# Optimization experiments

Hardware: AMD Instinct MI355X
Metric: run time of the kernel (lower is better)

## Reference

```python
import jax, jax.numpy as jnp
import numpy as np

B, S, D = 2, 2048, 2048
H, HKV, HD = 16, 2, 128
THETA = 10000.0


def setup_inputs() -> dict:
    key = jax.random.key(0)
    ks = jax.random.split(key, 5)
    x = jax.random.normal(ks[0], (B, S, D), jnp.float32)
    Wq = jax.random.normal(ks[1], (D, H * HD), jnp.float32) * 0.02
    Wk = jax.random.normal(ks[2], (D, HKV * HD), jnp.float32) * 0.02
    Wv = jax.random.normal(ks[3], (D, HKV * HD), jnp.float32) * 0.02
    Wo = jax.random.normal(ks[4], (H * HD, D), jnp.float32) * 0.02
    mask = jnp.tril(jnp.ones((S, S), jnp.int32))[None, None]  # causal [1,1,S,S]
    return {"x": x, "mask": mask, "Wq": Wq, "Wk": Wk, "Wv": Wv, "Wo": Wo}


def _rope(t, seq_len):
    # t: [B, S, H, HD]; matches RotaryPositionalEmbedding (cos/sin broadcast [S,1,HD])
    inv_freq = 1.0 / (THETA ** (jnp.arange(0, HD, 2, dtype=jnp.float32) / HD))
    pos = jnp.arange(seq_len, dtype=jnp.float32)
    freqs = jnp.einsum('i,j->ij', pos, inv_freq)          # [S, HD/2]
    emb = jnp.concatenate([freqs, freqs], axis=-1)        # [S, HD]
    cos = jnp.cos(emb)[:, None, :]
    sin = jnp.sin(emb)[:, None, :]
    x1, x2 = jnp.split(t, 2, axis=-1)
    rot = jnp.concatenate([-x2, x1], axis=-1)             # rotate_half
    return t * cos + rot * sin


def reference(x, mask, Wq, Wk, Wv, Wo):
    Bx, Sx, _ = x.shape
    q = (x @ Wq).reshape(Bx, Sx, H, HD)
    k = (x @ Wk).reshape(Bx, Sx, HKV, HD)
    v = (x @ Wv).reshape(Bx, Sx, HKV, HD)
    q = _rope(q, Sx)
    k = _rope(k, Sx)
    rep = H // HKV
    # torch .repeat along head dim == tiling (not interleaved)
    k = jnp.tile(k, (1, 1, rep, 1))  # [B, S, H, HD]
    v = jnp.tile(v, (1, 1, rep, 1))
    scale = 1.0 / np.sqrt(HD).astype(np.float32)
    scores = jnp.einsum('bqhd,bkhd->bhqk', q, k) * scale  # [B, H, S, S]
    scores = jnp.where(mask == 0, -jnp.inf, scores)
    attn = jax.nn.softmax(scores.astype(jnp.float32), axis=-1).astype(scores.dtype)
    out = jnp.einsum('bhqk,bkhd->bqhd', attn, v).reshape(Bx, Sx, H * HD)
    return out @ Wo
```

## Files before the change

### kernel.cpp

```cpp
#include <hip/hip_runtime.h>
#include <hip/hip_bf16.h>

#define S_LEN 2048
#define DMODEL 2048
#define NHEAD 16
#define NKVH 2
#define HDIM 128
#define NROW 4096
#define NQKV 2560
#define SCALE 0.08838834764831845f

using short8 = __attribute__((ext_vector_type(8))) short;
using bf16x8 = __attribute__((ext_vector_type(8))) __bf16;
using f32x4  = __attribute__((ext_vector_type(4))) float;

__device__ __forceinline__ f32x4 mfma16(short8 a, short8 b, f32x4 c) {
  return __builtin_amdgcn_mfma_f32_16x16x32_bf16(
      __builtin_bit_cast(bf16x8, a), __builtin_bit_cast(bf16x8, b), c, 0, 0, 0);
}

__device__ __forceinline__ void gload_lds16(const void* g, void* l) {
  __builtin_amdgcn_global_load_lds(
      (const __attribute__((address_space(1))) unsigned int*)g,
      (__attribute__((address_space(3))) unsigned int*)l, 16, 0, 0);
}

__device__ __forceinline__ void storeC(float* C, long idx, float v) { C[idx] = v; }
__device__ __forceinline__ void storeC(__hip_bfloat16* C, long idx, float v) {
  C[idx] = __float2bfloat16(v);
}

__device__ __forceinline__ unsigned short bf16bits(float f) {
  __hip_bfloat16 h = __float2bfloat16(f);
  return *(unsigned short*)&h;
}

__global__ void conv_x(const float* __restrict__ x, __hip_bfloat16* __restrict__ xb) {
  long i = ((long)blockIdx.x * 256 + threadIdx.x) * 4;
  float4 v = *(const float4*)(x + i);
  __hip_bfloat16 o[4];
  o[0] = __float2bfloat16(v.x); o[1] = __float2bfloat16(v.y);
  o[2] = __float2bfloat16(v.z); o[3] = __float2bfloat16(v.w);
  *(ushort4*)(xb + i) = *(const ushort4*)o;
}

__global__ void convT3(const float* __restrict__ Wq, const float* __restrict__ Wk,
                       const float* __restrict__ Wv, __hip_bfloat16* __restrict__ dst) {
  __shared__ float t[32][33];
  int nt = blockIdx.x, kt = blockIdx.y;
  int tx = threadIdx.x, ty = threadIdx.y;
  const float* src; int Ns, n0, row_off;
  if (nt < 64)      { src = Wq; Ns = 2048; n0 = nt * 32;        row_off = n0; }
  else if (nt < 72) { src = Wk; Ns = 256;  n0 = (nt - 64) * 32; row_off = 2048 + n0; }
  else              { src = Wv; Ns = 256;  n0 = (nt - 72) * 32; row_off = 2304 + n0; }
#pragma unroll
  for (int i = 0; i < 4; i++)
    t[ty + i * 8][tx] = src[(long)(kt * 32 + ty + i * 8) * Ns + n0 + tx];
  __syncthreads();
#pragma unroll
  for (int i = 0; i < 4; i++)
    dst[(long)(row_off + ty + i * 8) * 2048 + kt * 32 + tx] =
        __float2bfloat16(t[tx][ty + i * 8]);
}

__global__ void convT(const float* __restrict__ src, __hip_bfloat16* __restrict__ dst,
                      int Ns, int row_off) {
  __shared__ float t[32][33];
  int nt = blockIdx.x, kt = blockIdx.y;
  int tx = threadIdx.x, ty = threadIdx.y;
#pragma unroll
  for (int i = 0; i < 4; i++)
    t[ty + i * 8][tx] = src[(long)(kt * 32 + ty + i * 8) * Ns + nt * 32 + tx];
  __syncthreads();
#pragma unroll
  for (int i = 0; i < 4; i++)
    dst[(long)(row_off + nt * 32 + ty + i * 8) * 2048 + kt * 32 + tx] =
        __float2bfloat16(t[tx][ty + i * 8]);
}

__global__ void mk_table(float* __restrict__ cost, float* __restrict__ sint) {
  int i = blockIdx.x * 256 + threadIdx.x;
  int s = i >> 6, j = i & 63;
  double f = pow(10000.0, -(double)j / 64.0);
  double a = (double)s * f;
  cost[i] = (float)cos(a);
  sint[i] = (float)sin(a);
}

template <typename OutT>
__global__ void gemm_bt(const __hip_bfloat16* __restrict__ A,
                        const __hip_bfloat16* __restrict__ Bt,
                        OutT* __restrict__ C, int M, int N, int K) {
  __shared__ __align__(16) __hip_bfloat16 a_lds[128 * 32];
  __shared__ __align__(16) __hip_bfloat16 b_lds[128 * 32];
  const int tid = threadIdx.x;
  const int wid = tid >> 6, lane = tid & 63;
  const int m0 = blockIdx.y * 128, n0 = blockIdx.x * 128;
  const int wr = wid >> 1, wc = wid & 1;
  const int lrow = lane & 15, lk = lane >> 4;

  const __hip_bfloat16* ag0 = A + (long)(m0 + wid * 16 + (lane >> 2)) * K + (lane & 3) * 8;
  const __hip_bfloat16* bg0 = Bt + (long)(n0 + wid * 16 + (lane >> 2)) * K + (lane & 3) * 8;
  char* al = (char*)a_lds + wid * 1024 + lane * 16;
  char* bl = (char*)b_lds + wid * 1024 + lane * 16;

  f32x4 acc[4][4] = {};

  for (int k0 = 0; k0 < K; k0 += 32) {
    gload_lds16(ag0 + k0, al);
    gload_lds16(ag0 + 64 * (long)K + k0, al + 4096);
    gload_lds16(bg0 + k0, bl);
    gload_lds16(bg0 + 64 * (long)K + k0, bl + 4096);
    __syncthreads();
    short8 af[4], bfr[4];
#pragma unroll
    for (int mi = 0; mi < 4; mi++)
      af[mi] = *(const short8*)(a_lds + (wr * 64 + mi * 16 + lrow) * 32 + lk * 8);
#pragma unroll
    for (int ni = 0; ni < 4; ni++)
      bfr[ni] = *(const short8*)(b_lds + (wc * 64 + ni * 16 + lrow) * 32 + lk * 8);
#pragma unroll
    for (int mi = 0; mi < 4; mi++)
#pragma unroll
      for (int ni = 0; ni < 4; ni++)
        acc[mi][ni] = mfma16(af[mi], bfr[ni], acc[mi][ni]);
    __syncthreads();
  }
#pragma unroll
  for (int mi = 0; mi < 4; mi++)
#pragma unroll
    for (int ni = 0; ni < 4; ni++)
#pragma unroll
      for (int r = 0; r < 4; r++) {
        long row = m0 + wr * 64 + mi * 16 + lk * 4 + r;
        long col = n0 + wc * 64 + ni * 16 + lrow;
        storeC(C, row * N + col, acc[mi][ni][r]);
      }
}

__global__ void rope_kernel(const __hip_bfloat16* __restrict__ qkv,
                            const float* __restrict__ cost, const float* __restrict__ sint,
                            __hip_bfloat16* __restrict__ q_r, __hip_bfloat16* __restrict__ k_r) {
  int tid = threadIdx.x;
  long row = (long)blockIdx.x * 4 + (tid >> 6);
  int j = tid & 63;
  int hh = (int)(row % 18);
  long bs = row / 18;
  int s = (int)(bs & (S_LEN - 1));
  int b = (int)(bs >> 11);
  const __hip_bfloat16* src = qkv + bs * NQKV;
  float c = cost[s * 64 + j], sn = sint[s * 64 + j];
  int col0;
  float sc;
  __hip_bfloat16* dst;
  if (hh < NHEAD) {
    col0 = hh * HDIM;
    sc = SCALE;
    dst = q_r + ((long)(b * NHEAD + hh) * S_LEN + s) * HDIM;
  } else {
    int kv = hh - NHEAD;
    col0 = DMODEL + kv * HDIM;
    sc = 1.0f;
    dst = k_r + ((long)(b * NKVH + kv) * S_LEN + s) * HDIM;
  }
  float lo = __bfloat162float(src[col0 + j]);
  float hi = __bfloat162float(src[col0 + j + 64]);
  dst[j]      = __float2bfloat16((lo * c - hi * sn) * sc);
  dst[j + 64] = __float2bfloat16((hi * c + lo * sn) * sc);
}

__global__ void vtrans(const __hip_bfloat16* __restrict__ qkv, __hip_bfloat16* __restrict__ v_t) {
  __shared__ __hip_bfloat16 t[32][33];
  int st = blockIdx.x, dt = blockIdx.y, bk = blockIdx.z;
  int tx = threadIdx.x, ty = threadIdx.y;
#pragma unroll
  for (int i = 0; i < 4; i++)
    t[ty + i * 8][tx] = qkv[((long)(bk >> 1) * S_LEN + st * 32 + ty + i * 8) * NQKV +
                            DMODEL + NKVH * HDIM + (bk & 1) * HDIM + dt * 32 + tx];
  __syncthreads();
#pragma unroll
  for (int i = 0; i < 4; i++)
    v_t[((long)bk * HDIM + dt * 32 + ty + i * 8) * S_LEN + st * 32 + tx] = t[tx][ty + i * 8];
}

__global__ __launch_bounds__(512, 2) void attn_kernel(
    const __hip_bfloat16* __restrict__ q_r, const __hip_bfloat16* __restrict__ k_r,
    const __hip_bfloat16* __restrict__ v_t, __hip_bfloat16* __restrict__ attn_a) {
  __shared__ __align__(16) __hip_bfloat16 k_st[2][32 * 128];
  __shared__ __align__(16) __hip_bfloat16 v_st[2][128 * 32];
  __shared__ __align__(16) __hip_bfloat16 p_lds[8][16 * 40];
  const int tid = threadIdx.x;
  const int wid = tid >> 6, lane = tid & 63;
  const int lrow = lane & 15, lk = lane >> 4;
  const int bidx = blockIdx.x;
  const int qc0 = bidx & 63;
  const int kv = (bidx >> 6) & 1;
  const int b = bidx >> 7;
  const int h = kv + 2 * wid;

  const __hip_bfloat16* qb = q_r + (long)(b * NHEAD + h) * S_LEN * HDIM;
  const __hip_bfloat16* kb = k_r + (long)(b * NKVH + kv) * S_LEN * HDIM;
  const __hip_bfloat16* vb = v_t + (long)(b * NKVH + kv) * HDIM * S_LEN;

  const int krow = tid >> 4, kslot = tid & 15;
  const long kgoff = (long)krow * HDIM + ((kslot ^ (krow & 7)) << 3);
  const int vrow = tid >> 2, vslot = tid & 3;
  const long vgoff = (long)vrow * S_LEN + ((vslot ^ (vrow & 3)) << 3);
  char* kdst0 = (char*)&k_st[0][0] + tid * 16;
  char* kdst1 = (char*)&k_st[1][0] + tid * 16;
  char* vdst0 = (char*)&v_st[0][0] + tid * 16;
  char* vdst1 = (char*)&v_st[1][0] + tid * 16;

  for (int pass = 0; pass < 2; pass++) {
    const int qc = pass ? (127 - qc0) : qc0;
    const int q0 = qc * 16;
    const int nkt = (q0 + 15) / 32 + 1;

    short8 qf[4];
#pragma unroll
    for (int dc = 0; dc < 4; dc++)
      qf[dc] = *(const short8*)(qb + (long)(q0 + lrow) * HDIM + dc * 32 + lk * 8);

    f32x4 oacc[8] = {};
    float mrow = 4.0f;
    float lsum = 0.f;

    gload_lds16(kb + kgoff, kdst0);
    gload_lds16(vb + vgoff, vdst0);
    __syncthreads();

    for (int kt = 0; kt < nkt; kt++) {
      const int kc0 = kt * 32;
      const char* ks = (const char*)&k_st[kt & 1][0];
      const char* vs = (const char*)&v_st[kt & 1][0];
      if (kt + 1 < nkt) {
        gload_lds16(kb + kgoff + (long)(kc0 + 32) * HDIM, (kt & 1) ? kdst0 : kdst1);
        gload_lds16(vb + vgoff + (kc0 + 32), (kt & 1) ? vdst0 : vdst1);
      }
      short8 kf0[4], kf1[4];
      const int sw = lrow & 7;
#pragma unroll
      for (int dc = 0; dc < 4; dc++) {
        kf0[dc] = *(const short8*)(ks + lrow * 256 + (((dc * 4 + lk) ^ sw) << 4));
        kf1[dc] = *(const short8*)(ks + (16 + lrow) * 256 + (((dc * 4 + lk) ^ sw) << 4));
      }
      f32x4 s0 = {}, s1 = {};
#pragma unroll
      for (int dc = 0; dc < 4; dc++) {
        s0 = mfma16(kf0[dc], qf[dc], s0);
        s1 = mfma16(kf1[dc], qf[dc], s1);
      }
      short8 vf[8];
#pragma unroll
      for (int d2 = 0; d2 < 8; d2++) {
        int r = d2 * 16 + lrow;
        vf[d2] = *(const short8*)(vs + r * 64 + ((lk ^ (r & 3)) << 4));
      }
      float pv[8];
#pragma unroll
      for (int r = 0; r < 4; r++) { pv[r] = s0[r]; pv[4 + r] = s1[r]; }
      if (kt == nkt - 1) {
        int qrow = q0 + lrow;
#pragma unroll
        for (int cs = 0; cs < 2; cs++)
#pragma unroll
          for (int r = 0; r < 4; r++)
            if (kc0 + cs * 16 + lk * 4 + r > qrow) pv[cs * 4 + r] = -3.0e38f;
      }
      float mx = fmaxf(fmaxf(fmaxf(pv[0], pv[1]), fmaxf(pv[2], pv[3])),
                       fmaxf(fmaxf(pv[4], pv[5]), fmaxf(pv[6], pv[7])));
      if (__builtin_expect(__any(mx > mrow + 8.0f), 0)) {
        float mr = fmaxf(mx, __shfl_xor(mx, 16));
        mr = fmaxf(mr, __shfl_xor(mr, 32));
        float mnew = fmaxf(mrow, mr);
        float fr = __expf(mrow - mnew);
        lsum *= fr;
        mrow = mnew;
#pragma unroll
        for (int r2 = 0; r2 < 4; r2++) {
          float fro = __shfl(fr, lk * 4 + r2);
#pragma unroll
          for (int d2 = 0; d2 < 8; d2++) oacc[d2][r2] *= fro;
        }
      }
      float pe[8];
#pragma unroll
      for (int i = 0; i < 8; i++) pe[i] = __expf(pv[i] - mrow);
      lsum += ((pe[0] + pe[1]) + (pe[2] + pe[3])) + ((pe[4] + pe[5]) + (pe[6] + pe[7]));
      unsigned short pk[8];
#pragma unroll
      for (int i = 0; i < 8; i++) pk[i] = bf16bits(pe[i]);
      *(ushort4*)(&p_lds[wid][lrow * 40 + lk * 4]) = *(ushort4*)&pk[0];
      *(ushort4*)(&p_lds[wid][lrow * 40 + 16 + lk * 4]) = *(ushort4*)&pk[4];
      short8 pf = *(const short8*)(&p_lds[wid][lrow * 40 + lk * 8]);
#pragma unroll
      for (int d2 = 0; d2 < 8; d2++)
        oacc[d2] = mfma16(pf, vf[d2], oacc[d2]);
      __syncthreads();
    }
    float ls = lsum;
    ls += __shfl_xor(ls, 16);
    ls += __shfl_xor(ls, 32);
    float inv = 1.0f / ls;
#pragma unroll
    for (int r = 0; r < 4; r++) {
      float invr = __shfl(inv, lk * 4 + r);
      long row = (long)b * S_LEN + q0 + lk * 4 + r;
#pragma unroll
      for (int d2 = 0; d2 < 8; d2++)
        attn_a[row * DMODEL + h * HDIM + d2 * 16 + lrow] =
            __float2bfloat16(oacc[d2][r] * invr);
    }
  }
}

extern "C" void kernel_launch(void* const* d_in, const int* in_sizes, int n_in,
                              void* d_out, int out_size, void* d_ws, size_t ws_size,
                              hipStream_t stream) {
  const float* x  = (const float*)d_in[0];
  const float* Wq = (const float*)d_in[2];
  const float* Wk = (const float*)d_in[3];
  const float* Wv = (const float*)d_in[4];
  const float* Wo = (const float*)d_in[5];
  float* out = (float*)d_out;

  char* ws = (char*)d_ws;
  __hip_bfloat16* xb     = (__hip_bfloat16*)(ws + 0);
  __hip_bfloat16* attn_a = xb;
  __hip_bfloat16* wt1    = (__hip_bfloat16*)(ws + 16777216);
  __hip_bfloat16* wto    = (__hip_bfloat16*)(ws + 27262976);
  __hip_bfloat16* qkv    = (__hip_bfloat16*)(ws + 35651584);
  __hip_bfloat16* q_r    = (__hip_bfloat16*)(ws + 56623104);
  __hip_bfloat16* k_r    = (__hip_bfloat16*)(ws + 73400320);
  __hip_bfloat16* v_t    = (__hip_bfloat16*)(ws + 75497472);
  float* cost            = (float*)(ws + 77594624);
  float* sint            = (float*)(ws + 78118912);

  conv_x<<<8192, 256, 0, stream>>>(x, xb);
  convT3<<<dim3(80, 64), dim3(32, 8), 0, stream>>>(Wq, Wk, Wv, wt1);
  convT<<<dim3(64, 64), dim3(32, 8), 0, stream>>>(Wo, wto, 2048, 0);
  mk_table<<<512, 256, 0, stream>>>(cost, sint);

  gemm_bt<__hip_bfloat16><<<dim3(20, 32), 256, 0, stream>>>(xb, wt1, qkv, NROW, NQKV, DMODEL);

  rope_kernel<<<18432, 256, 0, stream>>>(qkv, cost, sint, q_r, k_r);
  vtrans<<<dim3(64, 4, 4), dim3(32, 8), 0, stream>>>(qkv, v_t);

  attn_kernel<<<256, 512, 0, stream>>>(q_r, k_r, v_t, attn_a);

  gemm_bt<float><<<dim3(16, 32), 256, 0, stream>>>(attn_a, wto, out, NROW, DMODEL, DMODEL);
}
```

Baseline: 202.6 us.

## Pre-tile K/V into MFMA fragment order, triple-buffer attention, remap GEMM blocks

The rope and V-transpose kernels now write K and V in a layout that matches the MFMA fragment order, so each 32-key tile is one contiguous 8KB chunk. The attention kernel loads these chunks linearly and reads fragments without swizzle. It also merges the two query passes into one continuous loop over a 3-deep LDS ring buffer, using explicit vmcnt waits and a single barrier per tile, so prefetch continues across the pass boundary. The GEMM also remaps block IDs in groups of 8 to change how tiles are spread for cache locality. The cost is extra LDS per block and more complex index math in the rope and vtrans stores.

```diff
diff --git a/kernel.cpp b/kernel.cpp
--- a/kernel.cpp
+++ b/kernel.cpp
@@ -95,7 +95,11 @@
   __shared__ __align__(16) __hip_bfloat16 b_lds[128 * 32];
   const int tid = threadIdx.x;
   const int wid = tid >> 6, lane = tid & 63;
-  const int m0 = blockIdx.y * 128, n0 = blockIdx.x * 128;
+  const int nbx = gridDim.x;
+  int bid = blockIdx.y * nbx + blockIdx.x;
+  const int nwg = nbx * gridDim.y;
+  bid = (bid & 7) * (nwg >> 3) + (bid >> 3);
+  const int m0 = (bid / nbx) * 128, n0 = (bid % nbx) * 128;
   const int wr = wid >> 1, wc = wid & 1;
   const int lrow = lane & 15, lk = lane >> 4;
 
@@ -140,7 +144,7 @@
 
 __global__ void rope_kernel(const __hip_bfloat16* __restrict__ qkv,
                             const float* __restrict__ cost, const float* __restrict__ sint,
-                            __hip_bfloat16* __restrict__ q_r, __hip_bfloat16* __restrict__ k_r) {
+                            __hip_bfloat16* __restrict__ q_r, __hip_bfloat16* __restrict__ k_t) {
   int tid = threadIdx.x;
   long row = (long)blockIdx.x * 4 + (tid >> 6);
   int j = tid & 63;
@@ -150,23 +154,26 @@
   int b = (int)(bs >> 11);
   const __hip_bfloat16* src = qkv + bs * NQKV;
   float c = cost[s * 64 + j], sn = sint[s * 64 + j];
-  int col0;
-  float sc;
-  __hip_bfloat16* dst;
   if (hh < NHEAD) {
-    col0 = hh * HDIM;
-    sc = SCALE;
-    dst = q_r + ((long)(b * NHEAD + hh) * S_LEN + s) * HDIM;
+    int col0 = hh * HDIM;
+    float lo = __bfloat162float(src[col0 + j]);
+    float hi = __bfloat162float(src[col0 + j + 64]);
+    __hip_bfloat16* dst = q_r + ((long)(b * NHEAD + hh) * S_LEN + s) * HDIM;
+    dst[j]      = __float2bfloat16((lo * c - hi * sn) * SCALE);
+    dst[j + 64] = __float2bfloat16((hi * c + lo * sn) * SCALE);
   } else {
-    int kv = hh - NHEAD;
-    col0 = DMODEL + kv * HDIM;
-    sc = 1.0f;
-    dst = k_r + ((long)(b * NKVH + kv) * S_LEN + s) * HDIM;
+    int kvh = hh - NHEAD;
+    int col0 = DMODEL + kvh * HDIM;
+    float lo = __bfloat162float(src[col0 + j]);
+    float hi = __bfloat162float(src[col0 + j + 64]);
+    long tb = (long)(b * NKVH + kvh) * (S_LEN * HDIM) + (long)(s >> 5) * 4096 +
+              (s & 15) * 8 + (j & 7);
+    int cs4 = ((s >> 4) & 1) * 4;
+    int lkq = ((j >> 3) & 3) * 16;
+    int dch = j >> 5;
+    k_t[tb + (long)((cs4 + dch) * 64 + lkq) * 8]     = __float2bfloat16(lo * c - hi * sn);
+    k_t[tb + (long)((cs4 + dch + 2) * 64 + lkq) * 8] = __float2bfloat16(hi * c + lo * sn);
   }
-  float lo = __bfloat162float(src[col0 + j]);
-  float hi = __bfloat162float(src[col0 + j + 64]);
-  dst[j]      = __float2bfloat16((lo * c - hi * sn) * sc);
-  dst[j + 64] = __float2bfloat16((hi * c + lo * sn) * sc);
 }
 
 __global__ void vtrans(const __hip_bfloat16* __restrict__ qkv, __hip_bfloat16* __restrict__ v_t) {
@@ -178,126 +185,54 @@
     t[ty + i * 8][tx] = qkv[((long)(bk >> 1) * S_LEN + st * 32 + ty + i * 8) * NQKV +
                             DMODEL + NKVH * HDIM + (bk & 1) * HDIM + dt * 32 + tx];
   __syncthreads();
-#pragma unroll
-  for (int i = 0; i < 4; i++)
-    v_t[((long)bk * HDIM + dt * 32 + ty + i * 8) * S_LEN + st * 32 + tx] = t[tx][ty + i * 8];
+  long base = (long)bk * (S_LEN * HDIM) + (long)st * 4096 + (tx >> 3) * 128 + (tx & 7);
+#pragma unroll
+  for (int i = 0; i < 4; i++) {
+    int d = dt * 32 + ty + i * 8;
+    v_t[base + (long)((d >> 4) * 64 + (d & 15)) * 8] = t[tx][ty + i * 8];
+  }
 }
 
 __global__ __launch_bounds__(512, 2) void attn_kernel(
-    const __hip_bfloat16* __restrict__ q_r, const __hip_bfloat16* __restrict__ k_r,
+    const __hip_bfloat16* __restrict__ q_r, const __hip_bfloat16* __restrict__ k_t,
     const __hip_bfloat16* __restrict__ v_t, __hip_bfloat16* __restrict__ attn_a) {
-  __shared__ __align__(16) __hip_bfloat16 k_st[2][32 * 128];
-  __shared__ __align__(16) __hip_bfloat16 v_st[2][128 * 32];
+  __shared__ __align__(16) __hip_bfloat16 k_st[3][4096];
+  __shared__ __align__(16) __hip_bfloat16 v_st[3][4096];
   __shared__ __align__(16) __hip_bfloat16 p_lds[8][16 * 40];
   const int tid = threadIdx.x;
   const int wid = tid >> 6, lane = tid & 63;
   const int lrow = lane & 15, lk = lane >> 4;
   const int bidx = blockIdx.x;
-  const int qc0 = bidx & 63;
+  const int c = bidx & 63;
   const int kv = (bidx >> 6) & 1;
   const int b = bidx >> 7;
   const int h = kv + 2 * wid;
 
+  const int nktA = (c >> 1) + 1;
+  const int cB = 127 - c;
+  const int NV = nktA + (cB >> 1) + 1;
+
   const __hip_bfloat16* qb = q_r + (long)(b * NHEAD + h) * S_LEN * HDIM;
-  const __hip_bfloat16* kb = k_r + (long)(b * NKVH + kv) * S_LEN * HDIM;
-  const __hip_bfloat16* vb = v_t + (long)(b * NKVH + kv) * HDIM * S_LEN;
-
-  const int krow = tid >> 4, kslot = tid & 15;
-  const long kgoff = (long)krow * HDIM + ((kslot ^ (krow & 7)) << 3);
-  const int vrow = tid >> 2, vslot = tid & 3;
-  const long vgoff = (long)vrow * S_LEN + ((vslot ^ (vrow & 3)) << 3);
-  char* kdst0 = (char*)&k_st[0][0] + tid * 16;
-  char* kdst1 = (char*)&k_st[1][0] + tid * 16;
-  char* vdst0 = (char*)&v_st[0][0] + tid * 16;
-  char* vdst1 = (char*)&v_st[1][0] + tid * 16;
-
-  for (int pass = 0; pass < 2; pass++) {
-    const int qc = pass ? (127 - qc0) : qc0;
-    const int q0 = qc * 16;
-    const int nkt = (q0 + 15) / 32 + 1;
-
-    short8 qf[4];
-#pragma unroll
-    for (int dc = 0; dc < 4; dc++)
-      qf[dc] = *(const short8*)(qb + (long)(q0 + lrow) * HDIM + dc * 32 + lk * 8);
-
-    f32x4 oacc[8] = {};
-    float mrow = 4.0f;
-    float lsum = 0.f;
-
-    gload_lds16(kb + kgoff, kdst0);
-    gload_lds16(vb + vgoff, vdst0);
-    __syncthreads();
-
-    for (int kt = 0; kt < nkt; kt++) {
-      const int kc0 = kt * 32;
-      const char* ks = (const char*)&k_st[kt & 1][0];
-      const char* vs = (const char*)&v_st[kt & 1][0];
-      if (kt + 1 < nkt) {
-        gload_lds16(kb + kgoff + (long)(kc0 + 32) * HDIM, (kt & 1) ? kdst0 : kdst1);
-        gload_lds16(vb + vgoff + (kc0 + 32), (kt & 1) ? vdst0 : vdst1);
-      }
-      short8 kf0[4], kf1[4];
-      const int sw = lrow & 7;
-#pragma unroll
-      for (int dc = 0; dc < 4; dc++) {
-        kf0[dc] = *(const short8*)(ks + lrow * 256 + (((dc * 4 + lk) ^ sw) << 4));
-        kf1[dc] = *(const short8*)(ks + (16 + lrow) * 256 + (((dc * 4 + lk) ^ sw) << 4));
-      }
-      f32x4 s0 = {}, s1 = {};
-#pragma unroll
-      for (int dc = 0; dc < 4; dc++) {
-        s0 = mfma16(kf0[dc], qf[dc], s0);
-        s1 = mfma16(kf1[dc], qf[dc], s1);
-      }
-      short8 vf[8];
-#pragma unroll
-      for (int d2 = 0; d2 < 8; d2++) {
-        int r = d2 * 16 + lrow;
-        vf[d2] = *(const short8*)(vs + r * 64 + ((lk ^ (r & 3)) << 4));
-      }
-      float pv[8];
-#pragma unroll
-      for (int r = 0; r < 4; r++) { pv[r] = s0[r]; pv[4 + r] = s1[r]; }
-      if (kt == nkt - 1) {
-        int qrow = q0 + lrow;
-#pragma unroll
-        for (int cs = 0; cs < 2; cs++)
-#pragma unroll
-          for (int r = 0; r < 4; r++)
-            if (kc0 + cs * 16 + lk * 4 + r > qrow) pv[cs * 4 + r] = -3.0e38f;
-      }
-      float mx = fmaxf(fmaxf(fmaxf(pv[0], pv[1]), fmaxf(pv[2], pv[3])),
-                       fmaxf(fmaxf(pv[4], pv[5]), fmaxf(pv[6], pv[7])));
-      if (__builtin_expect(__any(mx > mrow + 8.0f), 0)) {
-        float mr = fmaxf(mx, __shfl_xor(mx, 16));
-        mr = fmaxf(mr, __shfl_xor(mr, 32));
-        float mnew = fmaxf(mrow, mr);
-        float fr = __expf(mrow - mnew);
-        lsum *= fr;
-        mrow = mnew;
-#pragma unroll
-        for (int r2 = 0; r2 < 4; r2++) {
-          float fro = __shfl(fr, lk * 4 + r2);
-#pragma unroll
-          for (int d2 = 0; d2 < 8; d2++) oacc[d2][r2] *= fro;
-        }
-      }
-      float pe[8];
-#pragma unroll
-      for (int i = 0; i < 8; i++) pe[i] = __expf(pv[i] - mrow);
-      lsum += ((pe[0] + pe[1]) + (pe[2] + pe[3])) + ((pe[4] + pe[5]) + (pe[6] + pe[7]));
-      unsigned short pk[8];
-#pragma unroll
-      for (int i = 0; i < 8; i++) pk[i] = bf16bits(pe[i]);
-      *(ushort4*)(&p_lds[wid][lrow * 40 + lk * 4]) = *(ushort4*)&pk[0];
-      *(ushort4*)(&p_lds[wid][lrow * 40 + 16 + lk * 4]) = *(ushort4*)&pk[4];
-      short8 pf = *(const short8*)(&p_lds[wid][lrow * 40 + lk * 8]);
-#pragma unroll
-      for (int d2 = 0; d2 < 8; d2++)
-        oacc[d2] = mfma16(pf, vf[d2], oacc[d2]);
-      __syncthreads();
-    }
+  const __hip_bfloat16* kbase = k_t + (long)(b * NKVH + kv) * (S_LEN * HDIM);
+  const __hip_bfloat16* vbase = v_t + (long)(b * NKVH + kv) * (S_LEN * HDIM);
+
+  auto stage = [&](int tile, int bi) {
+    gload_lds16(kbase + (long)tile * 4096 + tid * 8, (char*)&k_st[bi][0] + tid * 16);
+    gload_lds16(vbase + (long)tile * 4096 + tid * 8, (char*)&v_st[bi][0] + tid * 16);
+  };
+  auto ptile = [&](int vt) { return vt < nktA ? vt : vt - nktA; };
+
+  int q0 = c * 16;
+  short8 qf[4];
+#pragma unroll
+  for (int dc = 0; dc < 4; dc++)
+    qf[dc] = *(const short8*)(qb + (long)(q0 + lrow) * HDIM + dc * 32 + lk * 8);
+
+  f32x4 oacc[8] = {};
+  float mrow = 4.0f;
+  float lsum = 0.f;
+
+  auto writeout = [&](int q0w) {
     float ls = lsum;
     ls += __shfl_xor(ls, 16);
     ls += __shfl_xor(ls, 32);
@@ -305,13 +240,104 @@
 #pragma unroll
     for (int r = 0; r < 4; r++) {
       float invr = __shfl(inv, lk * 4 + r);
-      long row = (long)b * S_LEN + q0 + lk * 4 + r;
+      long row = (long)b * S_LEN + q0w + lk * 4 + r;
 #pragma unroll
       for (int d2 = 0; d2 < 8; d2++)
         attn_a[row * DMODEL + h * HDIM + d2 * 16 + lrow] =
             __float2bfloat16(oacc[d2][r] * invr);
     }
+  };
+
+  stage(0, 0);
+  stage(ptile(1), 1);
+  int bi = 0;
+  for (int vt = 0; vt < NV; vt++) {
+    if (vt + 1 < NV) {
+      asm volatile("s_waitcnt vmcnt(2)" ::: "memory");
+    } else {
+      asm volatile("s_waitcnt vmcnt(0)" ::: "memory");
+    }
+    __builtin_amdgcn_s_barrier();
+    if (vt + 2 < NV) {
+      int b2 = bi + 2; if (b2 >= 3) b2 -= 3;
+      stage(ptile(vt + 2), b2);
+    }
+    const char* ks = (const char*)&k_st[bi][0];
+    const char* vs = (const char*)&v_st[bi][0];
+    const bool passA = vt < nktA;
+    const int kt = passA ? vt : vt - nktA;
+    const int kc0 = kt * 32;
+    const bool diag = passA ? (vt == nktA - 1) : (vt == NV - 1);
+
+    short8 kf0[4], kf1[4];
+#pragma unroll
+    for (int dc = 0; dc < 4; dc++) {
+      kf0[dc] = *(const short8*)(ks + (dc * 64 + lane) * 16);
+      kf1[dc] = *(const short8*)(ks + ((4 + dc) * 64 + lane) * 16);
+    }
+    f32x4 s0 = {}, s1 = {};
+#pragma unroll
+    for (int dc = 0; dc < 4; dc++) {
+      s0 = mfma16(kf0[dc], qf[dc], s0);
+      s1 = mfma16(kf1[dc], qf[dc], s1);
+    }
+    float pv[8];
+#pragma unroll
+    for (int r = 0; r < 4; r++) { pv[r] = s0[r]; pv[4 + r] = s1[r]; }
+    if (diag) {
+      int qrow = q0 + lrow;
+#pragma unroll
+      for (int cs = 0; cs < 2; cs++)
+#pragma unroll
+        for (int r = 0; r < 4; r++)
+          if (kc0 + cs * 16 + lk * 4 + r > qrow) pv[cs * 4 + r] = -3.0e38f;
+    }
+    float mx = fmaxf(fmaxf(fmaxf(pv[0], pv[1]), fmaxf(pv[2], pv[3])),
+                     fmaxf(fmaxf(pv[4], pv[5]), fmaxf(pv[6], pv[7])));
+    if (__builtin_expect(__any(mx > mrow + 8.0f), 0)) {
+      float mr = fmaxf(mx, __shfl_xor(mx, 16));
+      mr = fmaxf(mr, __shfl_xor(mr, 32));
+      float mnew = fmaxf(mrow, mr);
+      float fr = __expf(mrow - mnew);
+      lsum *= fr;
+      mrow = mnew;
+#pragma unroll
+      for (int r2 = 0; r2 < 4; r2++) {
+        float fro = __shfl(fr, lk * 4 + r2);
+#pragma unroll
+        for (int d2 = 0; d2 < 8; d2++) oacc[d2][r2] *= fro;
+      }
+    }
+    float pe[8];
+#pragma unroll
+    for (int i = 0; i < 8; i++) pe[i] = __expf(pv[i] - mrow);
+    lsum += ((pe[0] + pe[1]) + (pe[2] + pe[3])) + ((pe[4] + pe[5]) + (pe[6] + pe[7]));
+    unsigned short pk[8];
+#pragma unroll
+    for (int i = 0; i < 8; i++) pk[i] = bf16bits(pe[i]);
+    *(ushort4*)(&p_lds[wid][lrow * 40 + lk * 4]) = *(ushort4*)&pk[0];
+    *(ushort4*)(&p_lds[wid][lrow * 40 + 16 + lk * 4]) = *(ushort4*)&pk[4];
+    short8 pf = *(const short8*)(&p_lds[wid][lrow * 40 + lk * 8]);
+#pragma unroll
+    for (int d2 = 0; d2 < 8; d2++) {
+      short8 vf = *(const short8*)(vs + (d2 * 64 + lane) * 16);
+      oacc[d2] = mfma16(pf, vf, oacc[d2]);
+    }
+
+    if (vt == nktA - 1) {
+      writeout(q0);
+      q0 = cB * 16;
+#pragma unroll
+      for (int dc = 0; dc < 4; dc++)
+        qf[dc] = *(const short8*)(qb + (long)(q0 + lrow) * HDIM + dc * 32 + lk * 8);
+#pragma unroll
+      for (int d2 = 0; d2 < 8; d2++) oacc[d2] = f32x4{};
+      mrow = 4.0f;
+      lsum = 0.f;
+    }
+    bi = bi + 1; if (bi >= 3) bi -= 3;
   }
+  writeout(q0);
 }
 
 extern "C" void kernel_launch(void* const* d_in, const int* in_sizes, int n_in,
@@ -331,7 +357,7 @@
   __hip_bfloat16* wto    = (__hip_bfloat16*)(ws + 27262976);
   __hip_bfloat16* qkv    = (__hip_bfloat16*)(ws + 35651584);
   __hip_bfloat16* q_r    = (__hip_bfloat16*)(ws + 56623104);
-  __hip_bfloat16* k_r    = (__hip_bfloat16*)(ws + 73400320);
+  __hip_bfloat16* k_t    = (__hip_bfloat16*)(ws + 73400320);
   __hip_bfloat16* v_t    = (__hip_bfloat16*)(ws + 75497472);
   float* cost            = (float*)(ws + 77594624);
   float* sint            = (float*)(ws + 78118912);
@@ -343,10 +369,10 @@
 
   gemm_bt<__hip_bfloat16><<<dim3(20, 32), 256, 0, stream>>>(xb, wt1, qkv, NROW, NQKV, DMODEL);
 
-  rope_kernel<<<18432, 256, 0, stream>>>(qkv, cost, sint, q_r, k_r);
+  rope_kernel<<<18432, 256, 0, stream>>>(qkv, cost, sint, q_r, k_t);
   vtrans<<<dim3(64, 4, 4), dim3(32, 8), 0, stream>>>(qkv, v_t);
 
-  attn_kernel<<<256, 512, 0, stream>>>(q_r, k_r, v_t, attn_a);
+  attn_kernel<<<256, 512, 0, stream>>>(q_r, k_t, v_t, attn_a);
 
   gemm_bt<float><<<dim3(16, 32), 256, 0, stream>>>(attn_a, wto, out, NROW, DMODEL, DMODEL);
 }
```

Measured after the change: 209.8 us. +3.5%, slower.
